# Performance work log

Hardware: AMD Instinct MI355X
Metric: run time of the kernel (lower is better)

## Reference

```python
import jax, jax.numpy as jnp
import numpy as np

B, T, E = 8, 2048, 1024
H = 16
HD = E // H            # per-head hidden_dim = 64
DFF = 4 * E
DC = T // 512          # decay_constant = 4
EPS = 1e-5


def setup_inputs() -> dict:
    key = jax.random.key(0)
    ks = jax.random.split(key, 8)
    return {
        "x": jax.random.normal(ks[0], (B, T, E), jnp.float32),
        # per-head input projections (Linear(dim, hidden_dim) x H)
        "w_proj": jax.random.normal(ks[1], (H, E, HD), jnp.float32) / np.sqrt(E),
        "b_proj": jnp.zeros((H, HD), jnp.float32),
        # causal mixing weights: first H//2 heads are Col-repeat, last H//2 Row-repeat
        "mix_w": jax.random.normal(ks[2], (H, T), jnp.float32),
        "mix_b": jnp.zeros((H, T), jnp.float32),
        "decay": jnp.ones((H,), jnp.float32),   # decay_value params (init ones as in torch)
        "out_w": jax.random.normal(ks[3], (E, E), jnp.float32) / np.sqrt(E),
        "out_b": jnp.zeros((E,), jnp.float32),
        "ln1_g": jnp.ones((E,), jnp.float32),
        "ln1_b": jnp.zeros((E,), jnp.float32),
        "ln2_g": jnp.ones((E,), jnp.float32),
        "ln2_b": jnp.zeros((E,), jnp.float32),
        "ff_w1": jax.random.normal(ks[4], (E, DFF), jnp.float32) / np.sqrt(E),
        "ff_b1": jnp.zeros((DFF,), jnp.float32),
        "ff_w2": jax.random.normal(ks[5], (DFF, E), jnp.float32) / np.sqrt(DFF),
        "ff_b2": jnp.zeros((E,), jnp.float32),
        "index": 0,
    }


def _layernorm(x, g, b):
    mu = jnp.mean(x, -1, keepdims=True)
    var = jnp.var(x, -1, keepdims=True)
    return (x - mu) * jax.lax.rsqrt(var + EPS) * g + b


def _mix_matrices(mix_w, decay):
    # Col heads: M[i,j] = v[j] * d**((j-i)/DC) for j>=i else 0
    # Row heads: M[i,j] = v[i] * d**((j-i)/DC) for j>=i else 0
    i = jnp.arange(T)[:, None]
    j = jnp.arange(T)[None, :]
    d = jnp.clip(decay, 0.9, 1.0)                                   # (H,)
    expo = (j - i).astype(jnp.float32) / DC                         # (T,T)
    dec = d[:, None, None] ** expo                                  # (H,T,T)
    causal = (j >= i)
    half = H // 2
    Mcol = jnp.where(causal, mix_w[:half, None, :] * dec[:half], 0.0)
    Mrow = jnp.where(causal, mix_w[half:, :, None] * dec[half:], 0.0)
    return jnp.concatenate([Mcol, Mrow], axis=0)                    # (H,T,T)


def reference(x, w_proj, b_proj, mix_w, mix_b, decay, out_w, out_b,
              ln1_g, ln1_b, ln2_g, ln2_b, ff_w1, ff_b1, ff_w2, ff_b2, index):
    # ---- token-mixing sub-block (parallel path of MixedRepeatHeads) ----
    res = x
    h = _layernorm(x, ln1_g, ln1_b)
    # per-head projection: (B,T,E) x (H,E,HD) -> (B,H,T,HD)
    p = jnp.einsum('bte,hef->bhtf', h, w_proj) + b_proj[:, None, :]
    M = _mix_matrices(mix_w, decay)
    # causal decay mixing along time: out[b,h,s,f] = sum_t p[b,h,t,f] * M[h,t,s]
    mixed = jnp.einsum('bhtf,hts->bhsf', p, M) + mix_b[None, :, :, None]
    # concat heads along feature dim -> (B,T,E)
    mixed = mixed.transpose(0, 2, 1, 3).reshape(B, T, E)
    mixed = mixed @ out_w + out_b
    x = mixed + res
    # ---- feed-forward sub-block ----
    res = x
    h = _layernorm(x, ln2_g, ln2_b)
    h = jax.nn.gelu(h @ ff_w1 + ff_b1) @ ff_w2 + ff_b2
    return h + res
```

## Files before the change

kernel.cpp:

```cpp
#include <hip/hip_runtime.h>


#define TT 2048
#define EE 1024
#define HHD 64
#define MROWS 16384
#define SC_L 64

typedef __bf16 bf16x8 __attribute__((ext_vector_type(8)));
typedef float f32x4 __attribute__((ext_vector_type(4)));
typedef unsigned short u16;
typedef unsigned int u32;
typedef u16 u16x8 __attribute__((ext_vector_type(8)));

__device__ __forceinline__ u16 f2bf(float f) {
  u32 u = __builtin_bit_cast(u32, f);
  u += 0x7FFFu + ((u >> 16) & 1u);
  return (u16)(u >> 16);
}
__device__ __forceinline__ float bf2f(u16 s) {
  u32 u = ((u32)s) << 16;
  return __builtin_bit_cast(float, u);
}
__device__ __forceinline__ float gelu_f(float x) {
  float x2 = x * x;
  float e = -1.5957691216057308f * x * __builtin_fmaf(0.044715f, x2, 1.0f);
  return x * __builtin_amdgcn_rcpf(1.0f + __expf(e));
}
__device__ __forceinline__ void gload_lds16(const void* g, void* l) {
  __builtin_amdgcn_global_load_lds(
      (const __attribute__((address_space(1))) u32*)g,
      (__attribute__((address_space(3))) u32*)l, 16, 0, 0);
}
__device__ __forceinline__ void wg_barrier() {
  asm volatile("" ::: "memory");
  __builtin_amdgcn_s_barrier();
  asm volatile("" ::: "memory");
}

__global__ __launch_bounds__(256) void transpose_to_bf16(
    const float* __restrict__ src, u16* __restrict__ dst, int R, int C,
    long sbs, long dbs) {
  __shared__ float tile[32][33];
  src += (long)blockIdx.z * sbs;
  dst += (long)blockIdx.z * dbs;
  int c0 = blockIdx.x * 32, r0 = blockIdx.y * 32;
  int tx = threadIdx.x, ty = threadIdx.y;
#pragma unroll
  for (int i = 0; i < 4; i++)
    tile[ty + i * 8][tx] = src[(long)(r0 + ty + i * 8) * C + c0 + tx];
  __syncthreads();
#pragma unroll
  for (int i = 0; i < 4; i++)
    dst[(long)(c0 + ty + i * 8) * R + r0 + tx] = f2bf(tile[tx][ty + i * 8]);
}

__global__ __launch_bounds__(256) void ln_to_bf16(
    const float* __restrict__ x, const float* __restrict__ gam,
    const float* __restrict__ bet, u16* __restrict__ y) {
  int row = blockIdx.x;
  int tid = threadIdx.x;
  float4 v = ((const float4*)x)[row * 256 + tid];
  float s = v.x + v.y + v.z + v.w;
  float s2 = v.x * v.x + v.y * v.y + v.z * v.z + v.w * v.w;
#pragma unroll
  for (int off = 1; off < 64; off <<= 1) {
    s += __shfl_xor(s, off);
    s2 += __shfl_xor(s2, off);
  }
  __shared__ float red[8];
  int w = tid >> 6;
  if ((tid & 63) == 0) { red[w] = s; red[4 + w] = s2; }
  __syncthreads();
  s = red[0] + red[1] + red[2] + red[3];
  s2 = red[4] + red[5] + red[6] + red[7];
  float mu = s * (1.0f / 1024.0f);
  float var = s2 * (1.0f / 1024.0f) - mu * mu;
  float rstd = rsqrtf(var + 1e-5f);
  int e0 = tid * 4;
  ushort4 o;
  o.x = f2bf((v.x - mu) * rstd * gam[e0 + 0] + bet[e0 + 0]);
  o.y = f2bf((v.y - mu) * rstd * gam[e0 + 1] + bet[e0 + 1]);
  o.z = f2bf((v.z - mu) * rstd * gam[e0 + 2] + bet[e0 + 2]);
  o.w = f2bf((v.w - mu) * rstd * gam[e0 + 3] + bet[e0 + 3]);
  ((ushort4*)y)[row * 256 + tid] = o;
}

template <int EPI>
__global__ __launch_bounds__(512, 1) void gemm256q(
    const u16* __restrict__ A, const u16* __restrict__ Bt,
    const float* __restrict__ bias, const float* __restrict__ res, void* outp,
    int M, int N, int K, int px, int gxp, int byper) {
  __shared__ u16 lds[65536];
  const int tid = threadIdx.x;
  const int w = tid >> 6, lane = tid & 63;
  const int wm = w >> 2, wn = w & 3;
  const int l15 = lane & 15, lk = lane >> 4;

  const int gx = (int)gridDim.x;
  const int bid = (int)blockIdx.y * gx + (int)blockIdx.x;
  const int xcd = bid & 7, i = bid >> 3;
  const int bx = (xcd % gxp) * px + (i % px);
  const int by = (xcd / gxp) * byper + (i / px);
  const int m0 = by * 256, n0 = bx * 256;

  const int srow = w * 16 + (lane >> 2);
  const int gslot = (lane & 3) ^ ((srow >> 1) & 3);
  const u16* aS = A + (size_t)(m0 + srow) * K + gslot * 8;
  const u16* aS2 = A + (size_t)(m0 + 128 + srow) * K +
                   (((lane & 3) ^ (((128 + srow) >> 1) & 3)) * 8);
  const u16* bS = Bt + (size_t)(n0 + srow) * K + gslot * 8;
  const u16* bS2 = Bt + (size_t)(n0 + 128 + srow) * K +
                   (((lane & 3) ^ (((128 + srow) >> 1) & 3)) * 8);

  f32x4 acc[8][4];
  const f32x4 z = {0.f, 0.f, 0.f, 0.f};
#pragma unroll
  for (int mi = 0; mi < 8; mi++)
#pragma unroll
    for (int ni = 0; ni < 4; ni++) acc[mi][ni] = z;

  const int sl = (lk ^ ((l15 >> 1) & 3)) * 8;

#define STAGE(BUF, T_) { \
    u16* lb = lds + (BUF) * 16384 + w * 512; \
    const int kt = (T_) << 5; \
    gload_lds16(aS + kt, lb); \
    gload_lds16(aS2 + kt, lb + 4096); \
    gload_lds16(bS + kt, lb + 8192); \
    gload_lds16(bS2 + kt, lb + 12288); }

  const int nt = K >> 5;
  STAGE(0, 0);
  STAGE(1, 1);

  for (int t = 0; t < nt; ++t) {
    if (t + 2 < nt) {
      STAGE((t + 2) & 3, t + 2);
      asm volatile("s_waitcnt vmcnt(8)" ::: "memory");
    } else if (t + 1 < nt) {
      asm volatile("s_waitcnt vmcnt(4)" ::: "memory");
    } else {
      asm volatile("s_waitcnt vmcnt(0)" ::: "memory");
    }
    wg_barrier();

    const u16* lA = lds + (t & 3) * 16384;
    const u16* lB = lA + 8192;
    bf16x8 bq[4];
    {
      const u16* bp = lB + (wn * 64 + l15) * 32 + sl;
#pragma unroll
      for (int ni = 0; ni < 4; ni++) bq[ni] = *(const bf16x8*)(bp + ni * 512);
    }
    const u16* ap = lA + (wm * 128 + l15) * 32 + sl;
    __builtin_amdgcn_s_setprio(1);
#pragma unroll
    for (int mi = 0; mi < 8; mi++) {
      bf16x8 af = *(const bf16x8*)(ap + mi * 512);
#pragma unroll
      for (int ni = 0; ni < 4; ni++)
        acc[mi][ni] = __builtin_amdgcn_mfma_f32_16x16x32_bf16(af, bq[ni],
                                                              acc[mi][ni], 0, 0, 0);
    }
    __builtin_amdgcn_s_setprio(0);
  }
#undef STAGE

#pragma unroll
  for (int mi = 0; mi < 8; mi++) {
#pragma unroll
    for (int ni = 0; ni < 4; ni++) {
      int n = n0 + wn * 64 + ni * 16 + l15;
      float bvv = bias[n];
#pragma unroll
      for (int r = 0; r < 4; r++) {
        int m = m0 + wm * 128 + mi * 16 + lk * 4 + r;
        size_t idx = (size_t)m * N + n;
        float v = acc[mi][ni][r] + bvv;
        if (EPI == 0) {
          ((u16*)outp)[idx] = f2bf(v);
        } else if (EPI == 1) {
          ((float*)outp)[idx] = v + res[idx];
        } else {
          ((u16*)outp)[idx] = f2bf(gelu_f(v));
        }
      }
    }
  }
}

__global__ __launch_bounds__(64) void scan_carry(
    const u16* __restrict__ p, const float* __restrict__ mix_w,
    const float* __restrict__ decay, float* __restrict__ carry) {
  int chunk = blockIdx.x * 8 + (threadIdx.x >> 3);
  int fg = threadIdx.x & 7;
  int c = chunk & 31, h = (chunk >> 5) & 15, b = chunk >> 9;
  float d = fminf(fmaxf(decay[h], 0.9f), 1.0f);
  float r = powf(d, 0.25f);
  size_t base = (((size_t)b * TT + c * SC_L) * EE + h * HHD + fg * 8) >> 3;
  const u16x8* p8 = (const u16x8*)p;
  const float* mw = mix_w + h * TT + c * SC_L;
  bool isRow = (h >= 8);
  float S[8] = {0.f, 0.f, 0.f, 0.f, 0.f, 0.f, 0.f, 0.f};
  for (int t = 0; t < SC_L; t++) {
    u16x8 v = p8[base + (size_t)t * (EE / 8)];
    float wv = isRow ? mw[t] : 1.0f;
#pragma unroll
    for (int j = 0; j < 8; j++) S[j] = r * S[j] + wv * bf2f(v[j]);
  }
  float* cp = carry + chunk * 64 + fg * 8;
#pragma unroll
  for (int j = 0; j < 8; j++) cp[j] = S[j];
}

__global__ __launch_bounds__(64) void scan_apply(
    const u16* __restrict__ p, const float* __restrict__ mix_w,
    const float* __restrict__ mix_b, const float* __restrict__ decay,
    const float* __restrict__ carry, u16* __restrict__ mixed) {
  int chunk = blockIdx.x * 8 + (threadIdx.x >> 3);
  int fg = threadIdx.x & 7;
  int c = chunk & 31, h = (chunk >> 5) & 15, b = chunk >> 9;
  float d = fminf(fmaxf(decay[h], 0.9f), 1.0f);
  float r = powf(d, 0.25f);
  float rl = powf(r, (float)SC_L);
  int cb = chunk - c;
  float S[8] = {0.f, 0.f, 0.f, 0.f, 0.f, 0.f, 0.f, 0.f};
  for (int cc = 0; cc < c; cc++) {
    const float* cp = carry + (cb + cc) * 64 + fg * 8;
#pragma unroll
    for (int j = 0; j < 8; j++) S[j] = rl * S[j] + cp[j];
  }
  size_t base = (((size_t)b * TT + c * SC_L) * EE + h * HHD + fg * 8) >> 3;
  const u16x8* p8 = (const u16x8*)p;
  u16x8* m8 = (u16x8*)mixed;
  const float* mw = mix_w + h * TT + c * SC_L;
  const float* mb = mix_b + h * TT + c * SC_L;
  bool isRow = (h >= 8);
  for (int t = 0; t < SC_L; t++) {
    u16x8 v = p8[base + (size_t)t * (EE / 8)];
    float wq = isRow ? mw[t] : 1.0f;
    float wo = isRow ? 1.0f : mw[t];
    float bb = mb[t];
    u16x8 o;
#pragma unroll
    for (int j = 0; j < 8; j++) {
      S[j] = r * S[j] + wq * bf2f(v[j]);
      o[j] = f2bf(wo * S[j] + bb);
    }
    m8[base + (size_t)t * (EE / 8)] = o;
  }
}

extern "C" void kernel_launch(void* const* d_in, const int* in_sizes, int n_in,
                              void* d_out, int out_size, void* d_ws, size_t ws_size,
                              hipStream_t stream) {
  const float* x = (const float*)d_in[0];
  const float* w_proj = (const float*)d_in[1];
  const float* b_proj = (const float*)d_in[2];
  const float* mix_w = (const float*)d_in[3];
  const float* mix_b = (const float*)d_in[4];
  const float* decay = (const float*)d_in[5];
  const float* out_w = (const float*)d_in[6];
  const float* out_b = (const float*)d_in[7];
  const float* ln1_g = (const float*)d_in[8];
  const float* ln1_b = (const float*)d_in[9];
  const float* ln2_g = (const float*)d_in[10];
  const float* ln2_b = (const float*)d_in[11];
  const float* ff_w1 = (const float*)d_in[12];
  const float* ff_b1 = (const float*)d_in[13];
  const float* ff_w2 = (const float*)d_in[14];
  const float* ff_b2 = (const float*)d_in[15];
  float* out = (float*)d_out;

  char* ws = (char*)d_ws;
  const size_t MiB = 1ull << 20;
  u16* wWp = (u16*)(ws + 0 * MiB);
  u16* wWo = (u16*)(ws + 2 * MiB);
  u16* wW1 = (u16*)(ws + 4 * MiB);
  u16* wW2 = (u16*)(ws + 12 * MiB);
  u16* wMix = (u16*)(ws + 20 * MiB);
  u16* wH = (u16*)(ws + 52 * MiB);
  u16* wP = (u16*)(ws + 84 * MiB);
  u16* wU = (u16*)(ws + 52 * MiB);
  float* wCarry = (float*)(ws + 180 * MiB);

  dim3 tb(32, 8);
  transpose_to_bf16<<<dim3(2, 32, 16), tb, 0, stream>>>(w_proj, wWp, 1024, 64,
                                                        65536L, 65536L);
  transpose_to_bf16<<<dim3(32, 32, 1), tb, 0, stream>>>(out_w, wWo, 1024, 1024, 0L, 0L);
  transpose_to_bf16<<<dim3(128, 32, 1), tb, 0, stream>>>(ff_w1, wW1, 1024, 4096, 0L, 0L);
  transpose_to_bf16<<<dim3(32, 128, 1), tb, 0, stream>>>(ff_w2, wW2, 4096, 1024, 0L, 0L);

  ln_to_bf16<<<dim3(MROWS), dim3(256), 0, stream>>>(x, ln1_g, ln1_b, wH);

  gemm256q<0><<<dim3(4, 64), dim3(512), 0, stream>>>(
      wH, wWp, b_proj, (const float*)nullptr, (void*)wP, MROWS, 1024, 1024,
      4, 1, 8);

  scan_carry<<<dim3(512), dim3(64), 0, stream>>>(wP, mix_w, decay, wCarry);
  scan_apply<<<dim3(512), dim3(64), 0, stream>>>(wP, mix_w, mix_b, decay, wCarry, wMix);

  gemm256q<1><<<dim3(4, 64), dim3(512), 0, stream>>>(
      wMix, wWo, out_b, x, (void*)out, MROWS, 1024, 1024,
      4, 1, 8);

  ln_to_bf16<<<dim3(MROWS), dim3(256), 0, stream>>>(out, ln2_g, ln2_b, wMix);

  gemm256q<2><<<dim3(16, 64), dim3(512), 0, stream>>>(
      wMix, wW1, ff_b1, (const float*)nullptr, (void*)wU, MROWS, 4096, 1024,
      4, 4, 32);

  gemm256q<1><<<dim3(4, 64), dim3(512), 0, stream>>>(
      wU, wW2, ff_b2, out, (void*)out, MROWS, 1024, 4096,
      2, 2, 16);
}
```

Measured before the change: 520.4 us.

## Use direct global-to-register MFMA GEMM without LDS staging for FFN layers

Adds a GEMM kernel that loads A and B fragments straight from global memory into registers with double buffering, skipping the LDS tile staging used by gemm256q. It replaces the two feed-forward GEMMs with it. The aim is to remove LDS write/read traffic and barrier synchronisation. The cost is uncoalesced, strided global loads (16-byte per lane across rows), more reliance on L2/cache for reuse, and higher register pressure from 64 accumulators plus two fragment sets.

Result: slower. 961.7 us (+84.8%).

```diff
diff --git a/kernel.cpp b/kernel.cpp
--- a/kernel.cpp
+++ b/kernel.cpp
@@ -84,6 +84,95 @@
   o.z = f2bf((v.z - mu) * rstd * gam[e0 + 2] + bet[e0 + 2]);
   o.w = f2bf((v.w - mu) * rstd * gam[e0 + 3] + bet[e0 + 3]);
   ((ushort4*)y)[row * 256 + tid] = o;
+}
+
+template <int EPI>
+__global__ __launch_bounds__(512, 1) void gemm_dir(
+    const u16* __restrict__ A, const u16* __restrict__ Bt,
+    const float* __restrict__ bias, const float* __restrict__ res, void* outp,
+    int M, int N, int K, int px, int gxp, int byper) {
+  const int tid = threadIdx.x;
+  const int w = tid >> 6, lane = tid & 63;
+  const int wm = w >> 2, wn = w & 3;
+  const int l15 = lane & 15, lk = lane >> 4;
+
+  const int gx = (int)gridDim.x;
+  const int bid = (int)blockIdx.y * gx + (int)blockIdx.x;
+  const int xcd = bid & 7, i = bid >> 3;
+  const int bx = (xcd % gxp) * px + (i % px);
+  const int by = (xcd / gxp) * byper + (i / px);
+  const int m0 = by * 256, n0 = bx * 256;
+
+  const u16* aB = A + (size_t)(m0 + wm * 128 + l15) * K + lk * 8;
+  const u16* bB = Bt + (size_t)(n0 + wn * 64 + l15) * K + lk * 8;
+  const size_t rs16 = (size_t)16 * K;
+
+  f32x4 acc[8][4];
+  const f32x4 z = {0.f, 0.f, 0.f, 0.f};
+#pragma unroll
+  for (int mi = 0; mi < 8; mi++)
+#pragma unroll
+    for (int ni = 0; ni < 4; ni++) acc[mi][ni] = z;
+
+  bf16x8 a0[8], b0v[4], a1[8], b1v[4];
+
+#define LD_A(DST, KO) { \
+    _Pragma("unroll") \
+    for (int mi = 0; mi < 8; ++mi) \
+      DST[mi] = *(const bf16x8*)(aB + mi * rs16 + (KO)); }
+#define LD_B(DST, KO) { \
+    _Pragma("unroll") \
+    for (int ni = 0; ni < 4; ++ni) \
+      DST[ni] = *(const bf16x8*)(bB + ni * rs16 + (KO)); }
+#define MM(AV, BV) { \
+    __builtin_amdgcn_s_setprio(1); \
+    _Pragma("unroll") \
+    for (int mi = 0; mi < 8; ++mi) \
+      _Pragma("unroll") \
+      for (int ni = 0; ni < 4; ++ni) \
+        acc[mi][ni] = __builtin_amdgcn_mfma_f32_16x16x32_bf16( \
+            AV[mi], BV[ni], acc[mi][ni], 0, 0, 0); \
+    __builtin_amdgcn_s_setprio(0); }
+
+  LD_A(a0, 0);
+  LD_B(b0v, 0);
+  const int nk2 = K >> 6;
+  for (int kp = 0; kp < nk2; ++kp) {
+    const int kb = kp << 6;
+    LD_A(a1, kb + 32);
+    LD_B(b1v, kb + 32);
+    MM(a0, b0v);
+    if (kp + 1 < nk2) {
+      LD_A(a0, kb + 64);
+      LD_B(b0v, kb + 64);
+    }
+    MM(a1, b1v);
+  }
+#undef LD_A
+#undef LD_B
+#undef MM
+
+#pragma unroll
+  for (int mi = 0; mi < 8; mi++) {
+#pragma unroll
+    for (int ni = 0; ni < 4; ni++) {
+      int n = n0 + wn * 64 + ni * 16 + l15;
+      float bvv = bias[n];
+#pragma unroll
+      for (int r = 0; r < 4; r++) {
+        int m = m0 + wm * 128 + mi * 16 + lk * 4 + r;
+        size_t idx = (size_t)m * N + n;
+        float v = acc[mi][ni][r] + bvv;
+        if (EPI == 0) {
+          ((u16*)outp)[idx] = f2bf(v);
+        } else if (EPI == 1) {
+          ((float*)outp)[idx] = v + res[idx];
+        } else {
+          ((u16*)outp)[idx] = f2bf(gelu_f(v));
+        }
+      }
+    }
+  }
 }
 
 template <int EPI>
@@ -307,11 +396,11 @@
 
   ln_to_bf16<<<dim3(MROWS), dim3(256), 0, stream>>>(out, ln2_g, ln2_b, wMix);
 
-  gemm256q<2><<<dim3(16, 64), dim3(512), 0, stream>>>(
+  gemm_dir<2><<<dim3(16, 64), dim3(512), 0, stream>>>(
       wMix, wW1, ff_b1, (const float*)nullptr, (void*)wU, MROWS, 4096, 1024,
       4, 4, 32);
 
-  gemm256q<1><<<dim3(4, 64), dim3(512), 0, stream>>>(
+  gemm_dir<1><<<dim3(4, 64), dim3(512), 0, stream>>>(
       wU, wW2, ff_b2, out, (void*)out, MROWS, 1024, 4096,
       2, 2, 16);
 }
```
